# Kernel tuning notes

Hardware: AMD Instinct MI355X
Metric: run time of the kernel (lower is better)

## Reference

```python
import jax, jax.numpy as jnp
import numpy as np

RENDER_SIZE = 256   # renderer image_size
IMG_H, IMG_W = 480, 640
ORIG_SIZE = 640     # max(H, W)
SIGMA = 0.5         # soft-silhouette sharpness in pixels (approximates NR hard rasterizer)
CHUNK = 128         # faces per scan step (bounds peak memory)
N_VERTS = 2048
N_FACES = 4096


def _se3_exp(dof):
    """dof = [v(3), omega(3)] (pytorch3d order) -> (R [3,3], t [3]) column convention."""
    v, w = dof[:3], dof[3:]
    th2 = jnp.sum(w * w)
    th = jnp.sqrt(th2 + 1e-30)
    small = th < 1e-4
    th_s = jnp.where(small, 1.0, th)          # safe denom (avoids nan grads)
    th2_s = jnp.where(small, 1.0, th2)
    A = jnp.where(small, 1.0 - th2 / 6.0, jnp.sin(th_s) / th_s)
    B = jnp.where(small, 0.5 - th2 / 24.0, (1.0 - jnp.cos(th_s)) / th2_s)
    C = jnp.where(small, 1.0 / 6.0 - th2 / 120.0, (th_s - jnp.sin(th_s)) / (th2_s * th_s))
    Kx = jnp.array([[0.0, -w[2], w[1]], [w[2], 0.0, -w[0]], [-w[1], w[0], 0.0]], dtype=dof.dtype)
    K2 = Kx @ Kx
    I = jnp.eye(3, dtype=dof.dtype)
    R = I + A * Kx + B * K2
    V = I + B * Kx + C * K2   # left Jacobian
    return R, V @ v


def _cross2(u, w):
    return u[..., 0] * w[..., 1] - u[..., 1] * w[..., 0]


def _rasterize_silhouette(tri):
    """tri: [F,3,2] projected triangle verts in render-pixel coords -> [R,R] coverage."""
    P = RENDER_SIZE * RENDER_SIZE
    ys, xs = jnp.meshgrid(jnp.arange(RENDER_SIZE, dtype=jnp.float32) + 0.5,
                          jnp.arange(RENDER_SIZE, dtype=jnp.float32) + 0.5, indexing='ij')
    px, py = xs.reshape(-1), ys.reshape(-1)  # [P] pixel centers
    tris = tri.reshape(N_FACES // CHUNK, CHUNK, 3, 2)

    def body(logp, t3):
        a = t3                          # [C,3,2] edge start verts
        e = jnp.roll(t3, -1, axis=1) - a  # [C,3,2] edge vectors (v1-v0, v2-v1, v0-v2)
        area2 = _cross2(e[:, 0], -e[:, 2])            # signed doubled area, [C]
        sgn = jnp.where(area2 >= 0, 1.0, -1.0)        # winding fix so inside > 0
        elen = jnp.sqrt(jnp.sum(e * e, -1)) + 1e-9    # [C,3]
        c0 = e[..., 0] * a[..., 1] - e[..., 1] * a[..., 0]  # [C,3]
        # signed distance of each pixel to each edge line: [P,C,3]
        d = (e[None, :, :, 0] * py[:, None, None] - e[None, :, :, 1] * px[:, None, None] - c0[None]) / elen[None]
        d = sgn[None, :, None] * d
        dmin = jnp.min(d, axis=2)                     # [P,C] min edge distance
        s = jnp.minimum(jax.nn.sigmoid(dmin / SIGMA), 1.0 - 1e-6)
        return logp + jnp.sum(jnp.log1p(-s), axis=1), None

    logp, _ = jax.lax.scan(body, jnp.zeros(P, jnp.float32), tris)
    return (1.0 - jnp.exp(logp)).reshape(RENDER_SIZE, RENDER_SIZE)


def _resize_nearest(img, size):
    return jax.image.resize(img, (size, size), method='nearest')


def reference(dof, vertices, faces, K, mask_gt):
    R, t = _se3_exp(dof)
    cam = vertices @ R.T + t              # [N,3] camera coords
    uvw = cam @ K.T                       # pinhole projection
    xy = uvw[:, :2] / uvw[:, 2:3]         # pixel coords at orig_size resolution
    xy = xy * (RENDER_SIZE / ORIG_SIZE)   # scale to render grid
    tri = xy[faces]                       # [F,3,2]
    si = _rasterize_silhouette(tri)       # [R,R]
    si = _resize_nearest(si, ORIG_SIZE)[:IMG_H, :IMG_W]
    loss = jnp.sum((si - mask_gt) ** 2)
    return loss, si


def setup_inputs() -> dict:
    key = jax.random.key(0)
    k1, k2, k3, k4 = jax.random.split(key, 4)
    v = jax.random.normal(k1, (N_VERTS, 3), dtype=jnp.float32)
    vertices = 0.5 * v / (jnp.linalg.norm(v, axis=1, keepdims=True) + 1e-8)  # unit-ish sphere mesh
    faces = jax.random.randint(k2, (N_FACES, 3), 0, N_VERTS, dtype=jnp.int32)
    # pose: object ~2.5m in front of camera, small rotation + noise
    dof = jnp.array([0.0, 0.0, 2.5, 0.2, -0.1, 0.15], dtype=jnp.float32) \
          + 0.05 * jax.random.normal(k3, (6,), dtype=jnp.float32)
    K = jnp.array([[600.0, 0.0, 320.0], [0.0, 600.0, 240.0], [0.0, 0.0, 1.0]], dtype=jnp.float32)
    mask_gt = (jax.random.uniform(k4, (IMG_H, IMG_W)) < 0.3).astype(jnp.float32)
    return {"dof": dof, "vertices": vertices, "faces": faces, "K": K, "mask_gt": mask_gt}
```

## Files before the change

### kernel.cpp

```cpp
#include <hip/hip_runtime.h>
#include <math.h>

#define RENDER 256
#define IMG_H 480
#define IMG_W 640
#define NV 2048
#define NF 4096
#define FACE_SLICES 16
#define FACES_PER_SLICE (NF / FACE_SLICES)
#define TILES 256
#define N_UNITS (TILES * FACE_SLICES)

#define SIGMA_INV 2.0f
#define CAP 13.815510557964274f
#define LOG2E 1.4426950408889634f
#define LN2 0.6931471805599453f
#define ZK 2.8853900817779268f
#define CAP2 19.931568569324174f
#define THR_CAP2  50.8f
#define THR_SKIP2 -56.6f

#define WS_FD_OFF    0
#define WS_LOGP_OFF  (192 * 1024)

__global__ __launch_bounds__(256) void k_prep(const float* __restrict__ dof,
                                              const float* __restrict__ verts,
                                              const int* __restrict__ faces,
                                              const float* __restrict__ Km,
                                              float* __restrict__ fdata,
                                              float* __restrict__ logp,
                                              float* __restrict__ out) {
    if (blockIdx.x >= 16) {
        logp[(blockIdx.x - 16) * 256 + threadIdx.x] = 0.0f;
        if (blockIdx.x == 16 && threadIdx.x == 0) out[0] = 0.0f;
        return;
    }

    __shared__ float sxy[NV * 2];

    float v0 = dof[0], v1 = dof[1], v2 = dof[2];
    float w0 = dof[3], w1 = dof[4], w2 = dof[5];
    float th2 = w0 * w0 + w1 * w1 + w2 * w2;
    float th = sqrtf(th2 + 1e-30f);
    bool small = th < 1e-4f;
    float th_s = small ? 1.0f : th;
    float th2_s = small ? 1.0f : th2;
    float A = small ? (1.0f - th2 / 6.0f) : (sinf(th_s) / th_s);
    float B = small ? (0.5f - th2 / 24.0f) : ((1.0f - cosf(th_s)) / th2_s);
    float C = small ? (1.0f / 6.0f - th2 / 120.0f)
                    : ((th_s - sinf(th_s)) / (th2_s * th_s));
    float Kx[9] = {0.0f, -w2, w1, w2, 0.0f, -w0, -w1, w0, 0.0f};
    float w[3] = {w0, w1, w2};
    float R[9], V[9];
    for (int i = 0; i < 3; i++)
        for (int j = 0; j < 3; j++) {
            float K2 = w[i] * w[j] - (i == j ? th2 : 0.0f);
            float id = (i == j) ? 1.0f : 0.0f;
            R[i * 3 + j] = id + A * Kx[i * 3 + j] + B * K2;
            V[i * 3 + j] = id + B * Kx[i * 3 + j] + C * K2;
        }
    float t0 = V[0] * v0 + V[1] * v1 + V[2] * v2;
    float t1 = V[3] * v0 + V[4] * v1 + V[5] * v2;
    float t2 = V[6] * v0 + V[7] * v1 + V[8] * v2;
    float K00 = Km[0], K01 = Km[1], K02 = Km[2];
    float K10 = Km[3], K11 = Km[4], K12 = Km[5];
    float K20 = Km[6], K21 = Km[7], K22 = Km[8];
    const float scale = 256.0f / 640.0f;

    for (int n = threadIdx.x; n < NV; n += 256) {
        float vx = verts[n * 3], vy = verts[n * 3 + 1], vz = verts[n * 3 + 2];
        float cx = R[0] * vx + R[1] * vy + R[2] * vz + t0;
        float cy = R[3] * vx + R[4] * vy + R[5] * vz + t1;
        float cz = R[6] * vx + R[7] * vy + R[8] * vz + t2;
        float u = K00 * cx + K01 * cy + K02 * cz;
        float v = K10 * cx + K11 * cy + K12 * cz;
        float ww = K20 * cx + K21 * cy + K22 * cz;
        float rw = __builtin_amdgcn_rcpf(ww) * scale;
        sxy[n * 2]     = u * rw;
        sxy[n * 2 + 1] = v * rw;
    }
    __syncthreads();

    int f = blockIdx.x * 256 + threadIdx.x;
    int i0 = faces[f * 3], i1 = faces[f * 3 + 1], i2 = faces[f * 3 + 2];
    float x0 = sxy[i0 * 2], y0 = sxy[i0 * 2 + 1];
    float x1 = sxy[i1 * 2], y1 = sxy[i1 * 2 + 1];
    float x2 = sxy[i2 * 2], y2 = sxy[i2 * 2 + 1];
    float ex[3] = {x1 - x0, x2 - x1, x0 - x2};
    float ey[3] = {y1 - y0, y2 - y1, y0 - y2};
    float ax[3] = {x0, x1, x2};
    float ay[3] = {y0, y1, y2};
    float area2 = ex[0] * (-ey[2]) - ey[0] * (-ex[2]);
    float sgn = (area2 >= 0.0f) ? 1.0f : -1.0f;
    float* o = fdata + f * 12;
    for (int k = 0; k < 3; k++) {
        float elen = sqrtf(ex[k] * ex[k] + ey[k] * ey[k]) + 1e-9f;
        float c0 = ex[k] * ay[k] - ey[k] * ax[k];
        float inv = sgn / elen * ZK;
        o[k * 4 + 0] = ex[k] * inv;
        o[k * 4 + 1] = -ey[k] * inv;
        o[k * 4 + 2] = -c0 * inv;
        o[k * 4 + 3] = 0.0f;
    }
}

__global__ __launch_bounds__(256) void k_raster(const float* __restrict__ fdata,
                                                float* __restrict__ logp) {
    __shared__ float s_data[4096];
    __shared__ int s_n;
    __shared__ int s_ncap;
    const int tid = threadIdx.x;
    if (tid == 0) { s_n = 0; s_ncap = 0; }
    __syncthreads();

    const int unit = (blockIdx.x * 2053) & (N_UNITS - 1);
    const int tile = unit >> 4;
    const int slice = unit & 15;
    const int tileX = tile & 15;
    const int tileY = tile >> 4;
    const float cx = tileX * 16 + 8.0f;
    const float cy = tileY * 16 + 8.0f;
    const float4* __restrict__ fd4 = (const float4*)fdata;

    {
        int f = slice * FACES_PER_SLICE + tid;
        float4 e0 = fd4[f * 3 + 0];
        float4 e1 = fd4[f * 3 + 1];
        float4 e2 = fd4[f * 3 + 2];
        float d0 = fmaf(e0.y, cx, fmaf(e0.x, cy, e0.z));
        float d1 = fmaf(e1.y, cx, fmaf(e1.x, cy, e1.z));
        float d2 = fmaf(e2.y, cx, fmaf(e2.x, cy, e2.z));
        float dmin = fminf(d0, fminf(d1, d2));
        bool capped = dmin > THR_CAP2;
        bool live = (!capped) && (dmin > THR_SKIP2);
        unsigned long long mcap = __ballot(capped);
        unsigned long long mliv = __ballot(live);
        int lane = tid & 63;
        int base = 0;
        if (lane == 0) {
            base = atomicAdd(&s_n, __popcll(mliv));
            atomicAdd(&s_ncap, __popcll(mcap));
        }
        base = __shfl(base, 0, 64);
        if (live) {
            int pos = base + __popcll(mliv & ((1ull << lane) - 1ull));
            float4* dst = (float4*)(s_data + pos * 12);
            dst[0] = e0; dst[1] = e1; dst[2] = e2;
        }
    }
    __syncthreads();

    const int n = s_n;
    const int ncap = s_ncap;
    if (n == 0 && ncap == 0) return;

    const int wv = tid >> 6;
    const int lane = tid & 63;
    const int row = lane >> 2;
    const int col0 = lane & 3;
    const float py = (float)(tileY * 16 + row) + 0.5f;
    const float px0 = (float)(tileX * 16 + col0) + 0.5f;

    float acc[4] = {0.0f, 0.0f, 0.0f, 0.0f};
    const float4* sd = (const float4*)s_data;
    if (wv < n) {
        float4 c0 = sd[wv * 3 + 0], c1 = sd[wv * 3 + 1], c2 = sd[wv * 3 + 2];
        for (int i = wv; i < n; i += 4) {
            float4 n0 = sd[(i + 4) * 3 + 0];
            float4 n1 = sd[(i + 4) * 3 + 1];
            float4 n2 = sd[(i + 4) * 3 + 2];
            float t0 = fmaf(c0.x, py, c0.z);
            float t1 = fmaf(c1.x, py, c1.z);
            float t2 = fmaf(c2.x, py, c2.z);
            #pragma unroll
            for (int k = 0; k < 4; ++k) {
                float px = px0 + (float)(4 * k);
                float z = fminf(fmaf(c0.y, px, t0),
                          fminf(fmaf(c1.y, px, t1), fmaf(c2.y, px, t2)));
                float e = __builtin_amdgcn_exp2f(z);
                float sp2 = __builtin_amdgcn_logf(1.0f + e);
                acc[k] -= fminf(sp2, CAP2);
            }
            c0 = n0; c1 = n1; c2 = n2;
        }
    }

    __syncthreads();
    {
        int base = wv * 1024 + row * 16 + col0;
        s_data[base + 0]  = acc[0];
        s_data[base + 4]  = acc[1];
        s_data[base + 8]  = acc[2];
        s_data[base + 12] = acc[3];
    }
    __syncthreads();
    {
        int p = tid;
        float v = s_data[p] + s_data[1024 + p] + s_data[2048 + p] +
                  s_data[3072 + p] - CAP2 * (float)ncap;
        int iyp = tileY * 16 + (p >> 4);
        int ixp = tileX * 16 + (p & 15);
        atomicAdd(&logp[iyp * RENDER + ixp], v);
    }
}

__global__ __launch_bounds__(256) void k_final(const float* __restrict__ logp,
                                               const float* __restrict__ mask,
                                               float* __restrict__ out) {
    int idx = blockIdx.x * 256 + threadIdx.x;
    int r = idx / IMG_W;
    int c = idx - r * IMG_W;
    int ir = (2 * r + 1) / 5;
    int ic = (2 * c + 1) / 5;
    float si = 1.0f - __builtin_amdgcn_exp2f(logp[ir * RENDER + ic]);
    out[1 + idx] = si;
    float diff = si - mask[idx];
    float d2 = diff * diff;
    #pragma unroll
    for (int off = 32; off > 0; off >>= 1) d2 += __shfl_down(d2, off, 64);
    __shared__ float sred[4];
    int lane = threadIdx.x & 63;
    int wv = threadIdx.x >> 6;
    if (lane == 0) sred[wv] = d2;
    __syncthreads();
    if (threadIdx.x == 0)
        atomicAdd(out, sred[0] + sred[1] + sred[2] + sred[3]);
}

extern "C" void kernel_launch(void* const* d_in, const int* in_sizes, int n_in,
                              void* d_out, int out_size, void* d_ws, size_t ws_size,
                              hipStream_t stream) {
    const float* dof   = (const float*)d_in[0];
    const float* verts = (const float*)d_in[1];
    const int*   faces = (const int*)d_in[2];
    const float* Km    = (const float*)d_in[3];
    const float* mask  = (const float*)d_in[4];
    float* out = (float*)d_out;

    char* ws = (char*)d_ws;
    float* fdata = (float*)(ws + WS_FD_OFF);
    float* logp  = (float*)(ws + WS_LOGP_OFF);

    k_prep<<<272, 256, 0, stream>>>(dof, verts, faces, Km, fdata, logp, out);
    k_raster<<<N_UNITS, 256, 0, stream>>>(fdata, logp);
    k_final<<<(IMG_H * IMG_W) / 256, 256, 0, stream>>>(logp, mask, out);
}
```

Measured before the change: 104.8 us.

## Fuse vertex projection and face setup into raster kernel, replace atomics with per-slice partials

```diff
diff --git a/kernel.cpp b/kernel.cpp
--- a/kernel.cpp
+++ b/kernel.cpp
@@ -14,29 +14,25 @@
 #define SIGMA_INV 2.0f
 #define CAP 13.815510557964274f
 #define LOG2E 1.4426950408889634f
-#define LN2 0.6931471805599453f
 #define ZK 2.8853900817779268f
 #define CAP2 19.931568569324174f
 #define THR_CAP2  50.8f
 #define THR_SKIP2 -56.6f
 
-#define WS_FD_OFF    0
-#define WS_LOGP_OFF  (192 * 1024)
-
-__global__ __launch_bounds__(256) void k_prep(const float* __restrict__ dof,
-                                              const float* __restrict__ verts,
-                                              const int* __restrict__ faces,
-                                              const float* __restrict__ Km,
-                                              float* __restrict__ fdata,
-                                              float* __restrict__ logp,
-                                              float* __restrict__ out) {
-    if (blockIdx.x >= 16) {
-        logp[(blockIdx.x - 16) * 256 + threadIdx.x] = 0.0f;
-        if (blockIdx.x == 16 && threadIdx.x == 0) out[0] = 0.0f;
-        return;
-    }
-
-    __shared__ float sxy[NV * 2];
+#define WS_PARTS_OFF 0
+
+__global__ __launch_bounds__(256) void k_raster(const float* __restrict__ dof,
+                                                const float* __restrict__ verts,
+                                                const int* __restrict__ faces,
+                                                const float* __restrict__ Km,
+                                                float* __restrict__ parts,
+                                                float* __restrict__ out) {
+    __shared__ float s_buf[4096];
+    __shared__ int s_n;
+    __shared__ int s_ncap;
+    const int tid = threadIdx.x;
+    if (tid == 0) { s_n = 0; s_ncap = 0; }
+    if (blockIdx.x == 0 && tid == 0) out[0] = 0.0f;
 
     float v0 = dof[0], v1 = dof[1], v2 = dof[2];
     float w0 = dof[3], w1 = dof[4], w2 = dof[5];
@@ -67,50 +63,18 @@
     float K20 = Km[6], K21 = Km[7], K22 = Km[8];
     const float scale = 256.0f / 640.0f;
 
-    for (int n = threadIdx.x; n < NV; n += 256) {
+    for (int n = tid; n < NV; n += 256) {
         float vx = verts[n * 3], vy = verts[n * 3 + 1], vz = verts[n * 3 + 2];
-        float cx = R[0] * vx + R[1] * vy + R[2] * vz + t0;
-        float cy = R[3] * vx + R[4] * vy + R[5] * vz + t1;
-        float cz = R[6] * vx + R[7] * vy + R[8] * vz + t2;
-        float u = K00 * cx + K01 * cy + K02 * cz;
-        float v = K10 * cx + K11 * cy + K12 * cz;
-        float ww = K20 * cx + K21 * cy + K22 * cz;
+        float cxv = R[0] * vx + R[1] * vy + R[2] * vz + t0;
+        float cyv = R[3] * vx + R[4] * vy + R[5] * vz + t1;
+        float czv = R[6] * vx + R[7] * vy + R[8] * vz + t2;
+        float u = K00 * cxv + K01 * cyv + K02 * czv;
+        float v = K10 * cxv + K11 * cyv + K12 * czv;
+        float ww = K20 * cxv + K21 * cyv + K22 * czv;
         float rw = __builtin_amdgcn_rcpf(ww) * scale;
-        sxy[n * 2]     = u * rw;
-        sxy[n * 2 + 1] = v * rw;
-    }
-    __syncthreads();
-
-    int f = blockIdx.x * 256 + threadIdx.x;
-    int i0 = faces[f * 3], i1 = faces[f * 3 + 1], i2 = faces[f * 3 + 2];
-    float x0 = sxy[i0 * 2], y0 = sxy[i0 * 2 + 1];
-    float x1 = sxy[i1 * 2], y1 = sxy[i1 * 2 + 1];
-    float x2 = sxy[i2 * 2], y2 = sxy[i2 * 2 + 1];
-    float ex[3] = {x1 - x0, x2 - x1, x0 - x2};
-    float ey[3] = {y1 - y0, y2 - y1, y0 - y2};
-    float ax[3] = {x0, x1, x2};
-    float ay[3] = {y0, y1, y2};
-    float area2 = ex[0] * (-ey[2]) - ey[0] * (-ex[2]);
-    float sgn = (area2 >= 0.0f) ? 1.0f : -1.0f;
-    float* o = fdata + f * 12;
-    for (int k = 0; k < 3; k++) {
-        float elen = sqrtf(ex[k] * ex[k] + ey[k] * ey[k]) + 1e-9f;
-        float c0 = ex[k] * ay[k] - ey[k] * ax[k];
-        float inv = sgn / elen * ZK;
-        o[k * 4 + 0] = ex[k] * inv;
-        o[k * 4 + 1] = -ey[k] * inv;
-        o[k * 4 + 2] = -c0 * inv;
-        o[k * 4 + 3] = 0.0f;
-    }
-}
-
-__global__ __launch_bounds__(256) void k_raster(const float* __restrict__ fdata,
-                                                float* __restrict__ logp) {
-    __shared__ float s_data[4096];
-    __shared__ int s_n;
-    __shared__ int s_ncap;
-    const int tid = threadIdx.x;
-    if (tid == 0) { s_n = 0; s_ncap = 0; }
+        s_buf[n * 2]     = u * rw;
+        s_buf[n * 2 + 1] = v * rw;
+    }
     __syncthreads();
 
     const int unit = (blockIdx.x * 2053) & (N_UNITS - 1);
@@ -120,16 +84,36 @@
     const int tileY = tile >> 4;
     const float cx = tileX * 16 + 8.0f;
     const float cy = tileY * 16 + 8.0f;
-    const float4* __restrict__ fd4 = (const float4*)fdata;
-
+
+    float cA[3], cB[3], cC[3];
     {
         int f = slice * FACES_PER_SLICE + tid;
-        float4 e0 = fd4[f * 3 + 0];
-        float4 e1 = fd4[f * 3 + 1];
-        float4 e2 = fd4[f * 3 + 2];
-        float d0 = fmaf(e0.y, cx, fmaf(e0.x, cy, e0.z));
-        float d1 = fmaf(e1.y, cx, fmaf(e1.x, cy, e1.z));
-        float d2 = fmaf(e2.y, cx, fmaf(e2.x, cy, e2.z));
+        int i0 = faces[f * 3], i1 = faces[f * 3 + 1], i2 = faces[f * 3 + 2];
+        float x0 = s_buf[i0 * 2], y0 = s_buf[i0 * 2 + 1];
+        float x1 = s_buf[i1 * 2], y1 = s_buf[i1 * 2 + 1];
+        float x2 = s_buf[i2 * 2], y2 = s_buf[i2 * 2 + 1];
+        float ex[3] = {x1 - x0, x2 - x1, x0 - x2};
+        float ey[3] = {y1 - y0, y2 - y1, y0 - y2};
+        float ax[3] = {x0, x1, x2};
+        float ay[3] = {y0, y1, y2};
+        float area2 = ex[0] * (-ey[2]) - ey[0] * (-ex[2]);
+        float sgn = (area2 >= 0.0f) ? 1.0f : -1.0f;
+        #pragma unroll
+        for (int k = 0; k < 3; k++) {
+            float elen = sqrtf(ex[k] * ex[k] + ey[k] * ey[k]) + 1e-9f;
+            float c0 = ex[k] * ay[k] - ey[k] * ax[k];
+            float inv = sgn / elen * ZK;
+            cA[k] = ex[k] * inv;
+            cB[k] = -ey[k] * inv;
+            cC[k] = -c0 * inv;
+        }
+    }
+    __syncthreads();
+
+    {
+        float d0 = fmaf(cB[0], cx, fmaf(cA[0], cy, cC[0]));
+        float d1 = fmaf(cB[1], cx, fmaf(cA[1], cy, cC[1]));
+        float d2 = fmaf(cB[2], cx, fmaf(cA[2], cy, cC[2]));
         float dmin = fminf(d0, fminf(d1, d2));
         bool capped = dmin > THR_CAP2;
         bool live = (!capped) && (dmin > THR_SKIP2);
@@ -144,15 +128,16 @@
         base = __shfl(base, 0, 64);
         if (live) {
             int pos = base + __popcll(mliv & ((1ull << lane) - 1ull));
-            float4* dst = (float4*)(s_data + pos * 12);
-            dst[0] = e0; dst[1] = e1; dst[2] = e2;
+            float4* dst = (float4*)(s_buf + pos * 12);
+            dst[0] = make_float4(cA[0], cB[0], cC[0], 0.0f);
+            dst[1] = make_float4(cA[1], cB[1], cC[1], 0.0f);
+            dst[2] = make_float4(cA[2], cB[2], cC[2], 0.0f);
         }
     }
     __syncthreads();
 
     const int n = s_n;
     const int ncap = s_ncap;
-    if (n == 0 && ncap == 0) return;
 
     const int wv = tid >> 6;
     const int lane = tid & 63;
@@ -162,21 +147,21 @@
     const float px0 = (float)(tileX * 16 + col0) + 0.5f;
 
     float acc[4] = {0.0f, 0.0f, 0.0f, 0.0f};
-    const float4* sd = (const float4*)s_data;
+    const float4* sd = (const float4*)s_buf;
     if (wv < n) {
         float4 c0 = sd[wv * 3 + 0], c1 = sd[wv * 3 + 1], c2 = sd[wv * 3 + 2];
         for (int i = wv; i < n; i += 4) {
             float4 n0 = sd[(i + 4) * 3 + 0];
             float4 n1 = sd[(i + 4) * 3 + 1];
             float4 n2 = sd[(i + 4) * 3 + 2];
-            float t0 = fmaf(c0.x, py, c0.z);
-            float t1 = fmaf(c1.x, py, c1.z);
-            float t2 = fmaf(c2.x, py, c2.z);
+            float t0p = fmaf(c0.x, py, c0.z);
+            float t1p = fmaf(c1.x, py, c1.z);
+            float t2p = fmaf(c2.x, py, c2.z);
             #pragma unroll
             for (int k = 0; k < 4; ++k) {
                 float px = px0 + (float)(4 * k);
-                float z = fminf(fmaf(c0.y, px, t0),
-                          fminf(fmaf(c1.y, px, t1), fmaf(c2.y, px, t2)));
+                float z = fminf(fmaf(c0.y, px, t0p),
+                          fminf(fmaf(c1.y, px, t1p), fmaf(c2.y, px, t2p)));
                 float e = __builtin_amdgcn_exp2f(z);
                 float sp2 = __builtin_amdgcn_logf(1.0f + e);
                 acc[k] -= fminf(sp2, CAP2);
@@ -188,23 +173,23 @@
     __syncthreads();
     {
         int base = wv * 1024 + row * 16 + col0;
-        s_data[base + 0]  = acc[0];
-        s_data[base + 4]  = acc[1];
-        s_data[base + 8]  = acc[2];
-        s_data[base + 12] = acc[3];
+        s_buf[base + 0]  = acc[0];
+        s_buf[base + 4]  = acc[1];
+        s_buf[base + 8]  = acc[2];
+        s_buf[base + 12] = acc[3];
     }
     __syncthreads();
     {
         int p = tid;
-        float v = s_data[p] + s_data[1024 + p] + s_data[2048 + p] +
-                  s_data[3072 + p] - CAP2 * (float)ncap;
+        float v = s_buf[p] + s_buf[1024 + p] + s_buf[2048 + p] +
+                  s_buf[3072 + p] - CAP2 * (float)ncap;
         int iyp = tileY * 16 + (p >> 4);
         int ixp = tileX * 16 + (p & 15);
-        atomicAdd(&logp[iyp * RENDER + ixp], v);
+        parts[slice * (RENDER * RENDER) + iyp * RENDER + ixp] = v;
     }
 }
 
-__global__ __launch_bounds__(256) void k_final(const float* __restrict__ logp,
+__global__ __launch_bounds__(256) void k_final(const float* __restrict__ parts,
                                                const float* __restrict__ mask,
                                                float* __restrict__ out) {
     int idx = blockIdx.x * 256 + threadIdx.x;
@@ -212,7 +197,12 @@
     int c = idx - r * IMG_W;
     int ir = (2 * r + 1) / 5;
     int ic = (2 * c + 1) / 5;
-    float si = 1.0f - __builtin_amdgcn_exp2f(logp[ir * RENDER + ic]);
+    int p = ir * RENDER + ic;
+    float lp = 0.0f;
+    #pragma unroll
+    for (int s = 0; s < FACE_SLICES; ++s)
+        lp += parts[s * (RENDER * RENDER) + p];
+    float si = 1.0f - __builtin_amdgcn_exp2f(lp);
     out[1 + idx] = si;
     float diff = si - mask[idx];
     float d2 = diff * diff;
@@ -237,11 +227,8 @@
     const float* mask  = (const float*)d_in[4];
     float* out = (float*)d_out;
 
-    char* ws = (char*)d_ws;
-    float* fdata = (float*)(ws + WS_FD_OFF);
-    float* logp  = (float*)(ws + WS_LOGP_OFF);
-
-    k_prep<<<272, 256, 0, stream>>>(dof, verts, faces, Km, fdata, logp, out);
-    k_raster<<<N_UNITS, 256, 0, stream>>>(fdata, logp);
-    k_final<<<(IMG_H * IMG_W) / 256, 256, 0, stream>>>(logp, mask, out);
+    float* parts = (float*)((char*)d_ws + WS_PARTS_OFF);
+
+    k_raster<<<N_UNITS, 256, 0, stream>>>(dof, verts, faces, Km, parts, out);
+    k_final<<<(IMG_H * IMG_W) / 256, 256, 0, stream>>>(parts, mask, out);
 }
```

New measurement: 116.2 us. 1.11x slower.

## Replace atomic logp accumulation with per-slice partial buffers reduced in final kernel

Applied to the files above, without the earlier changes.

```diff
diff --git a/kernel.cpp b/kernel.cpp
--- a/kernel.cpp
+++ b/kernel.cpp
@@ -14,27 +14,21 @@
 #define SIGMA_INV 2.0f
 #define CAP 13.815510557964274f
 #define LOG2E 1.4426950408889634f
-#define LN2 0.6931471805599453f
 #define ZK 2.8853900817779268f
 #define CAP2 19.931568569324174f
 #define THR_CAP2  50.8f
 #define THR_SKIP2 -56.6f
 
 #define WS_FD_OFF    0
-#define WS_LOGP_OFF  (192 * 1024)
+#define WS_PARTS_OFF (192 * 1024)
 
 __global__ __launch_bounds__(256) void k_prep(const float* __restrict__ dof,
                                               const float* __restrict__ verts,
                                               const int* __restrict__ faces,
                                               const float* __restrict__ Km,
                                               float* __restrict__ fdata,
-                                              float* __restrict__ logp,
                                               float* __restrict__ out) {
-    if (blockIdx.x >= 16) {
-        logp[(blockIdx.x - 16) * 256 + threadIdx.x] = 0.0f;
-        if (blockIdx.x == 16 && threadIdx.x == 0) out[0] = 0.0f;
-        return;
-    }
+    if (blockIdx.x == 0 && threadIdx.x == 0) out[0] = 0.0f;
 
     __shared__ float sxy[NV * 2];
 
@@ -105,8 +99,8 @@
 }
 
 __global__ __launch_bounds__(256) void k_raster(const float* __restrict__ fdata,
-                                                float* __restrict__ logp) {
-    __shared__ float s_data[4096];
+                                                float* __restrict__ parts) {
+    __shared__ float s_buf[4096];
     __shared__ int s_n;
     __shared__ int s_ncap;
     const int tid = threadIdx.x;
@@ -144,7 +138,7 @@
         base = __shfl(base, 0, 64);
         if (live) {
             int pos = base + __popcll(mliv & ((1ull << lane) - 1ull));
-            float4* dst = (float4*)(s_data + pos * 12);
+            float4* dst = (float4*)(s_buf + pos * 12);
             dst[0] = e0; dst[1] = e1; dst[2] = e2;
         }
     }
@@ -152,7 +146,6 @@
 
     const int n = s_n;
     const int ncap = s_ncap;
-    if (n == 0 && ncap == 0) return;
 
     const int wv = tid >> 6;
     const int lane = tid & 63;
@@ -162,21 +155,21 @@
     const float px0 = (float)(tileX * 16 + col0) + 0.5f;
 
     float acc[4] = {0.0f, 0.0f, 0.0f, 0.0f};
-    const float4* sd = (const float4*)s_data;
+    const float4* sd = (const float4*)s_buf;
     if (wv < n) {
         float4 c0 = sd[wv * 3 + 0], c1 = sd[wv * 3 + 1], c2 = sd[wv * 3 + 2];
         for (int i = wv; i < n; i += 4) {
             float4 n0 = sd[(i + 4) * 3 + 0];
             float4 n1 = sd[(i + 4) * 3 + 1];
             float4 n2 = sd[(i + 4) * 3 + 2];
-            float t0 = fmaf(c0.x, py, c0.z);
-            float t1 = fmaf(c1.x, py, c1.z);
-            float t2 = fmaf(c2.x, py, c2.z);
+            float t0p = fmaf(c0.x, py, c0.z);
+            float t1p = fmaf(c1.x, py, c1.z);
+            float t2p = fmaf(c2.x, py, c2.z);
             #pragma unroll
             for (int k = 0; k < 4; ++k) {
                 float px = px0 + (float)(4 * k);
-                float z = fminf(fmaf(c0.y, px, t0),
-                          fminf(fmaf(c1.y, px, t1), fmaf(c2.y, px, t2)));
+                float z = fminf(fmaf(c0.y, px, t0p),
+                          fminf(fmaf(c1.y, px, t1p), fmaf(c2.y, px, t2p)));
                 float e = __builtin_amdgcn_exp2f(z);
                 float sp2 = __builtin_amdgcn_logf(1.0f + e);
                 acc[k] -= fminf(sp2, CAP2);
@@ -188,23 +181,23 @@
     __syncthreads();
     {
         int base = wv * 1024 + row * 16 + col0;
-        s_data[base + 0]  = acc[0];
-        s_data[base + 4]  = acc[1];
-        s_data[base + 8]  = acc[2];
-        s_data[base + 12] = acc[3];
+        s_buf[base + 0]  = acc[0];
+        s_buf[base + 4]  = acc[1];
+        s_buf[base + 8]  = acc[2];
+        s_buf[base + 12] = acc[3];
     }
     __syncthreads();
     {
         int p = tid;
-        float v = s_data[p] + s_data[1024 + p] + s_data[2048 + p] +
-                  s_data[3072 + p] - CAP2 * (float)ncap;
+        float v = s_buf[p] + s_buf[1024 + p] + s_buf[2048 + p] +
+                  s_buf[3072 + p] - CAP2 * (float)ncap;
         int iyp = tileY * 16 + (p >> 4);
         int ixp = tileX * 16 + (p & 15);
-        atomicAdd(&logp[iyp * RENDER + ixp], v);
-    }
-}
-
-__global__ __launch_bounds__(256) void k_final(const float* __restrict__ logp,
+        parts[slice * (RENDER * RENDER) + iyp * RENDER + ixp] = v;
+    }
+}
+
+__global__ __launch_bounds__(256) void k_final(const float* __restrict__ parts,
                                                const float* __restrict__ mask,
                                                float* __restrict__ out) {
     int idx = blockIdx.x * 256 + threadIdx.x;
@@ -212,7 +205,12 @@
     int c = idx - r * IMG_W;
     int ir = (2 * r + 1) / 5;
     int ic = (2 * c + 1) / 5;
-    float si = 1.0f - __builtin_amdgcn_exp2f(logp[ir * RENDER + ic]);
+    int p = ir * RENDER + ic;
+    float lp = 0.0f;
+    #pragma unroll
+    for (int s = 0; s < FACE_SLICES; ++s)
+        lp += parts[s * (RENDER * RENDER) + p];
+    float si = 1.0f - __builtin_amdgcn_exp2f(lp);
     out[1 + idx] = si;
     float diff = si - mask[idx];
     float d2 = diff * diff;
@@ -239,9 +237,9 @@
 
     char* ws = (char*)d_ws;
     float* fdata = (float*)(ws + WS_FD_OFF);
-    float* logp  = (float*)(ws + WS_LOGP_OFF);
-
-    k_prep<<<272, 256, 0, stream>>>(dof, verts, faces, Km, fdata, logp, out);
-    k_raster<<<N_UNITS, 256, 0, stream>>>(fdata, logp);
-    k_final<<<(IMG_H * IMG_W) / 256, 256, 0, stream>>>(logp, mask, out);
-}
+    float* parts = (float*)(ws + WS_PARTS_OFF);
+
+    k_prep<<<16, 256, 0, stream>>>(dof, verts, faces, Km, fdata, out);
+    k_raster<<<N_UNITS, 256, 0, stream>>>(fdata, parts);
+    k_final<<<(IMG_H * IMG_W) / 256, 256, 0, stream>>>(parts, mask, out);
+}
```

New measurement: 108.3 us. 3.3% more time.
